# Kernel tuning notes

Measured on AMD Instinct MI355X. Metric: run time of the kernel, lower is better.

Reference implementation:

```python
import jax, jax.numpy as jnp
import numpy as np

EPS = 1e-6  # torch F.pairwise_distance default eps added to the difference


def setup_inputs() -> dict:
    key = jax.random.key(0)
    k1, k2 = jax.random.split(key)
    N, D = 8192, 256
    embeddings = jax.random.normal(k1, (N, D), dtype=jnp.float32)
    labels = jax.random.randint(k2, (N,), 0, 64, dtype=jnp.int32)
    return {"embeddings": embeddings, "labels": labels}


def reference(embeddings, labels):
    # Fused replacement for the O(N^2) python loop:
    # dist[i,j] = ||e_i - e_j + EPS||_2 (torch pairwise_distance semantics)
    #           = sqrt(||e_i||^2 + ||e_j||^2 - 2 e_i.e_j + 2*EPS*(sum(e_i)-sum(e_j)) + D*EPS^2)
    N, D = embeddings.shape
    sq_norm = jnp.sum(embeddings * embeddings, axis=-1)        # (N,)
    row_sum = jnp.sum(embeddings, axis=-1)                     # (N,)
    gram = embeddings @ embeddings.T                           # (N, N)
    sq = (sq_norm[:, None] + sq_norm[None, :] - 2.0 * gram
          + 2.0 * EPS * (row_sum[:, None] - row_sum[None, :])
          + D * EPS * EPS)
    dist = jnp.sqrt(jnp.maximum(sq, 0.0))                      # (N, N)
    mask = labels[:, None] == labels[None, :]                  # (N, N) bool
    loss = jnp.sum(jnp.where(mask, dist, 0.0)) / (N * (N - 1))
    return loss
```

## Files before the change

### kernel.cpp

```cpp
#include <hip/hip_runtime.h>
#include <stdint.h>


#define NROWS 8192
#define DDIM 256
#define NLAB 64
#define NTILEB (NLAB * 3)

typedef __attribute__((ext_vector_type(8))) short bfrag8;
typedef __attribute__((ext_vector_type(4))) float f32x4;

__device__ __forceinline__ unsigned short f2bf(float f) {
  unsigned u = __float_as_uint(f);
  u += 0x7FFFu + ((u >> 16) & 1u);
  return (unsigned short)(u >> 16);
}

__global__ void __launch_bounds__(512)
k_fused(const float* __restrict__ E, const int* __restrict__ lab,
        float* __restrict__ partials) {
  __shared__ __align__(16) char As[128 * 512];
  __shared__ __align__(16) char Bs[128 * 512];
  __shared__ int rowlistS[256];
  __shared__ float qAS[128], qBS[128];
  __shared__ int wcntS[8];
  __shared__ float wsum[8];

  const int bid = blockIdx.x;
  const int g = bid / 3, p = bid % 3;
  const int t = threadIdx.x, l = t & 63, w = t >> 6;
  const int tit = (p == 2) ? 1 : 0, tjt = (p == 0) ? 0 : 1;
  const bool diag = (p != 1);

  int lv[16];
  #pragma unroll
  for (int i = 0; i < 16; ++i)
    lv[i] = lab[(w * 16 + i) * 64 + l];

  int cntw = 0;
  #pragma unroll
  for (int i = 0; i < 16; ++i)
    cntw += (int)__popcll(__ballot(lv[i] == g));
  if (l == 0) wcntS[w] = cntw;
  if (t == 0) rowlistS[0] = 0;
  __syncthreads();
  int n_total = 0, base = 0;
  #pragma unroll
  for (int w2 = 0; w2 < 8; ++w2) {
    const int c = wcntS[w2];
    n_total += c;
    base += (w2 < w) ? c : 0;
  }
  #pragma unroll
  for (int i = 0; i < 16; ++i) {
    const unsigned long long m = __ballot(lv[i] == g);
    if (lv[i] == g) {
      const int rank = base + (int)__popcll(m & ((1ull << l) - 1ull));
      if (rank < 256) rowlistS[rank] = (w * 16 + i) * 64 + l;
    }
    base += (int)__popcll(m);
  }
  const int n = min(n_total, 256);
  __syncthreads();

  float blocksum = 0.f;
  const bool empty = (p != 0 && n <= 128);
  if (!empty) {
    const int gsw = l >> 1;
    const int half8 = (l & 1) * 8;
    if (diag) {
      #pragma unroll 8
      for (int r8 = 0; r8 < 16; ++r8) {
        const int r = w * 16 + r8;
        const int li = tit * 128 + r;
        const int grow = rowlistS[(li < n) ? li : 0];
        const float4 v = *reinterpret_cast<const float4*>(E + (size_t)grow * DDIM + l * 4);
        ushort4 b4;
        b4.x = f2bf(v.x); b4.y = f2bf(v.y); b4.z = f2bf(v.z); b4.w = f2bf(v.w);
        *reinterpret_cast<ushort4*>(
            As + r * 512 + ((gsw ^ (r & 15)) << 4) + half8) = b4;
      }
    } else {
      #pragma unroll 8
      for (int r8 = 0; r8 < 16; ++r8) {
        const int r = w * 16 + r8;
        const int growA = rowlistS[(r < n) ? r : 0];
        const int growB = rowlistS[(128 + r < n) ? 128 + r : 0];
        const float4 va = *reinterpret_cast<const float4*>(E + (size_t)growA * DDIM + l * 4);
        const float4 vb = *reinterpret_cast<const float4*>(E + (size_t)growB * DDIM + l * 4);
        ushort4 ba, bb;
        ba.x = f2bf(va.x); ba.y = f2bf(va.y); ba.z = f2bf(va.z); ba.w = f2bf(va.w);
        bb.x = f2bf(vb.x); bb.y = f2bf(vb.y); bb.z = f2bf(vb.z); bb.w = f2bf(vb.w);
        const int off = r * 512 + ((gsw ^ (r & 15)) << 4) + half8;
        *reinterpret_cast<ushort4*>(As + off) = ba;
        *reinterpret_cast<ushort4*>(Bs + off) = bb;
      }
    }
    __syncthreads();

    if (diag) {
      const int r = t >> 2, q4 = t & 3;
      float q = 0.f;
      #pragma unroll
      for (int i = 0; i < 8; ++i) {
        const int gidx = q4 * 8 + i;
        const bfrag8 v = *reinterpret_cast<const bfrag8*>(
            As + r * 512 + ((gidx ^ (r & 15)) << 4));
        #pragma unroll
        for (int e = 0; e < 8; ++e) {
          const float f = __uint_as_float(((unsigned)(unsigned short)v[e]) << 16);
          q = fmaf(f, f, q);
        }
      }
      q += __shfl_xor(q, 1);
      q += __shfl_xor(q, 2);
      if ((t & 3) == 0) qAS[r] = q;
    } else {
      const int rAll = t >> 1, hf = t & 1;
      const int r = rAll & 127;
      const char* buf = (rAll < 128) ? As : Bs;
      float q = 0.f;
      #pragma unroll
      for (int i = 0; i < 16; ++i) {
        const int gidx = hf * 16 + i;
        const bfrag8 v = *reinterpret_cast<const bfrag8*>(
            buf + r * 512 + ((gidx ^ (r & 15)) << 4));
        #pragma unroll
        for (int e = 0; e < 8; ++e) {
          const float f = __uint_as_float(((unsigned)(unsigned short)v[e]) << 16);
          q = fmaf(f, f, q);
        }
      }
      q += __shfl_xor(q, 1);
      if (hf == 0) { if (rAll < 128) qAS[r] = q; else qBS[r] = q; }
    }

    const char* Bbuf = diag ? As : Bs;
    const float* qBp = diag ? qAS : qBS;
    const int wr = w >> 2, wc = w & 3;
    const int colsel = l & 15;
    const int ksel = l >> 4;

    f32x4 acc[4][2];
    const f32x4 zero = {0.f, 0.f, 0.f, 0.f};
    #pragma unroll
    for (int m = 0; m < 4; ++m)
      #pragma unroll
      for (int nn = 0; nn < 2; ++nn)
        acc[m][nn] = zero;

    #pragma unroll
    for (int kk = 0; kk < 8; ++kk) {
      bfrag8 af[4], bf[2];
      #pragma unroll
      for (int m = 0; m < 4; ++m) {
        const int row = wr * 64 + m * 16 + colsel;
        const int gidx = (kk * 4 + ksel) ^ (row & 15);
        af[m] = *reinterpret_cast<const bfrag8*>(As + row * 512 + (gidx << 4));
      }
      #pragma unroll
      for (int nn = 0; nn < 2; ++nn) {
        const int row = wc * 32 + nn * 16 + colsel;
        const int gidx = (kk * 4 + ksel) ^ (row & 15);
        bf[nn] = *reinterpret_cast<const bfrag8*>(Bbuf + row * 512 + (gidx << 4));
      }
      #pragma unroll
      for (int m = 0; m < 4; ++m)
        #pragma unroll
        for (int nn = 0; nn < 2; ++nn)
          acc[m][nn] = __builtin_amdgcn_mfma_f32_16x16x32_bf16(af[m], bf[nn],
                                                               acc[m][nn], 0, 0, 0);
    }
    __syncthreads();

    float lsum = 0.f;
    #pragma unroll
    for (int m = 0; m < 4; ++m) {
      const int ib = wr * 64 + m * 16 + ksel * 4;
      const float q0 = qAS[ib], q1 = qAS[ib + 1], q2 = qAS[ib + 2], q3 = qAS[ib + 3];
      const int li = tit * 128 + ib;
      #pragma unroll
      for (int nn = 0; nn < 2; ++nn) {
        const int jb = wc * 32 + nn * 16 + colsel;
        const int lj = tjt * 128 + jb;
        const bool jv = lj < n;
        const float qj = qBp[jb];
        const f32x4 a = acc[m][nn];
        const float d0 = __builtin_amdgcn_sqrtf(fmaxf(q0 + qj - 2.f * a[0], 0.f));
        const float d1 = __builtin_amdgcn_sqrtf(fmaxf(q1 + qj - 2.f * a[1], 0.f));
        const float d2 = __builtin_amdgcn_sqrtf(fmaxf(q2 + qj - 2.f * a[2], 0.f));
        const float d3 = __builtin_amdgcn_sqrtf(fmaxf(q3 + qj - 2.f * a[3], 0.f));
        if (jv) {
          lsum += (li + 0 < n && li + 0 != lj) ? d0 : 0.f;
          lsum += (li + 1 < n && li + 1 != lj) ? d1 : 0.f;
          lsum += (li + 2 < n && li + 2 != lj) ? d2 : 0.f;
          lsum += (li + 3 < n && li + 3 != lj) ? d3 : 0.f;
        }
      }
    }
    #pragma unroll
    for (int o = 32; o; o >>= 1) lsum += __shfl_down(lsum, o);
    if (l == 0) wsum[w] = lsum;
    __syncthreads();
    const float wgt = (p == 1) ? 2.0f : 1.0f;
    blocksum = wgt * (wsum[0] + wsum[1] + wsum[2] + wsum[3] +
                      wsum[4] + wsum[5] + wsum[6] + wsum[7]);
  }

  if (t == 0) partials[bid] = blocksum;
}

__global__ void __launch_bounds__(64)
k_final(const float* __restrict__ partials, float* __restrict__ out, double invn) {
  const int l = threadIdx.x;
  double s = (double)partials[l] + (double)partials[l + 64] +
             (double)partials[l + 128];
  #pragma unroll
  for (int o = 32; o; o >>= 1) s += __shfl_down(s, o);
  if (l == 0) out[0] = (float)(s * invn);
}

extern "C" void kernel_launch(void* const* d_in, const int* in_sizes, int n_in,
                              void* d_out, int out_size, void* d_ws, size_t ws_size,
                              hipStream_t stream) {
  const float* E = (const float*)d_in[0];
  const int* lab = (const int*)d_in[1];
  float* out = (float*)d_out;
  (void)n_in; (void)in_sizes; (void)out_size; (void)ws_size;

  float* partials = (float*)d_ws;

  const double invn = 1.0 / ((double)NROWS * (double)(NROWS - 1));
  k_fused<<<NTILEB, 512, 0, stream>>>(E, lab, partials);
  k_final<<<1, 64, 0, stream>>>(partials, out, invn);
}
```

Before: 16.17 us.

## Split off-diagonal label tile across two blocks and fuse norms into staging

```diff
diff --git a/kernel.cpp b/kernel.cpp
--- a/kernel.cpp
+++ b/kernel.cpp
@@ -5,7 +5,7 @@
 #define NROWS 8192
 #define DDIM 256
 #define NLAB 64
-#define NTILEB (NLAB * 3)
+#define NBLK (NLAB * 4)
 
 typedef __attribute__((ext_vector_type(8))) short bfrag8;
 typedef __attribute__((ext_vector_type(4))) float f32x4;
@@ -14,6 +14,10 @@
   unsigned u = __float_as_uint(f);
   u += 0x7FFFu + ((u >> 16) & 1u);
   return (unsigned short)(u >> 16);
+}
+
+__device__ __forceinline__ float bf2f(unsigned short h) {
+  return __uint_as_float(((unsigned)h) << 16);
 }
 
 __global__ void __launch_bounds__(512)
@@ -27,10 +31,11 @@
   __shared__ float wsum[8];
 
   const int bid = blockIdx.x;
-  const int g = bid / 3, p = bid % 3;
+  const int g = bid >> 2, p = bid & 3;
   const int t = threadIdx.x, l = t & 63, w = t >> 6;
-  const int tit = (p == 2) ? 1 : 0, tjt = (p == 0) ? 0 : 1;
-  const bool diag = (p != 1);
+  const bool diag = (p < 2);
+  const int a0 = (p == 1) ? 128 : ((p == 3) ? 64 : 0);
+  const int b0 = (p == 0) ? 0 : 128;
 
   int lv[16];
   #pragma unroll
@@ -64,147 +69,188 @@
   __syncthreads();
 
   float blocksum = 0.f;
-  const bool empty = (p != 0 && n <= 128);
-  if (!empty) {
+  const bool active = (a0 < n) && (b0 < n);
+  if (active) {
     const int gsw = l >> 1;
     const int half8 = (l & 1) * 8;
     if (diag) {
       #pragma unroll 8
       for (int r8 = 0; r8 < 16; ++r8) {
         const int r = w * 16 + r8;
-        const int li = tit * 128 + r;
-        const int grow = rowlistS[(li < n) ? li : 0];
+        const int gi = a0 + r;
+        const int grow = rowlistS[(gi < n) ? gi : 0];
         const float4 v = *reinterpret_cast<const float4*>(E + (size_t)grow * DDIM + l * 4);
         ushort4 b4;
         b4.x = f2bf(v.x); b4.y = f2bf(v.y); b4.z = f2bf(v.z); b4.w = f2bf(v.w);
         *reinterpret_cast<ushort4*>(
             As + r * 512 + ((gsw ^ (r & 15)) << 4) + half8) = b4;
+        const float f0 = bf2f(b4.x), f1 = bf2f(b4.y);
+        const float f2 = bf2f(b4.z), f3 = bf2f(b4.w);
+        float q = f0 * f0 + f1 * f1 + f2 * f2 + f3 * f3;
+        #pragma unroll
+        for (int o = 32; o; o >>= 1) q += __shfl_down(q, o);
+        if (l == 0) qAS[r] = q;
       }
     } else {
+      #pragma unroll 8
+      for (int r8 = 0; r8 < 8; ++r8) {
+        const int r = w * 8 + r8;
+        const int gi = a0 + r;
+        const int grow = rowlistS[(gi < n) ? gi : 0];
+        const float4 v = *reinterpret_cast<const float4*>(E + (size_t)grow * DDIM + l * 4);
+        ushort4 b4;
+        b4.x = f2bf(v.x); b4.y = f2bf(v.y); b4.z = f2bf(v.z); b4.w = f2bf(v.w);
+        *reinterpret_cast<ushort4*>(
+            As + r * 512 + ((gsw ^ (r & 15)) << 4) + half8) = b4;
+        const float f0 = bf2f(b4.x), f1 = bf2f(b4.y);
+        const float f2 = bf2f(b4.z), f3 = bf2f(b4.w);
+        float q = f0 * f0 + f1 * f1 + f2 * f2 + f3 * f3;
+        #pragma unroll
+        for (int o = 32; o; o >>= 1) q += __shfl_down(q, o);
+        if (l == 0) qAS[r] = q;
+      }
       #pragma unroll 8
       for (int r8 = 0; r8 < 16; ++r8) {
         const int r = w * 16 + r8;
-        const int growA = rowlistS[(r < n) ? r : 0];
-        const int growB = rowlistS[(128 + r < n) ? 128 + r : 0];
-        const float4 va = *reinterpret_cast<const float4*>(E + (size_t)growA * DDIM + l * 4);
-        const float4 vb = *reinterpret_cast<const float4*>(E + (size_t)growB * DDIM + l * 4);
-        ushort4 ba, bb;
-        ba.x = f2bf(va.x); ba.y = f2bf(va.y); ba.z = f2bf(va.z); ba.w = f2bf(va.w);
-        bb.x = f2bf(vb.x); bb.y = f2bf(vb.y); bb.z = f2bf(vb.z); bb.w = f2bf(vb.w);
-        const int off = r * 512 + ((gsw ^ (r & 15)) << 4) + half8;
-        *reinterpret_cast<ushort4*>(As + off) = ba;
-        *reinterpret_cast<ushort4*>(Bs + off) = bb;
+        const int gj = 128 + r;
+        const int grow = rowlistS[(gj < n) ? gj : 0];
+        const float4 v = *reinterpret_cast<const float4*>(E + (size_t)grow * DDIM + l * 4);
+        ushort4 b4;
+        b4.x = f2bf(v.x); b4.y = f2bf(v.y); b4.z = f2bf(v.z); b4.w = f2bf(v.w);
+        *reinterpret_cast<ushort4*>(
+            Bs + r * 512 + ((gsw ^ (r & 15)) << 4) + half8) = b4;
+        const float f0 = bf2f(b4.x), f1 = bf2f(b4.y);
+        const float f2 = bf2f(b4.z), f3 = bf2f(b4.w);
+        float q = f0 * f0 + f1 * f1 + f2 * f2 + f3 * f3;
+        #pragma unroll
+        for (int o = 32; o; o >>= 1) q += __shfl_down(q, o);
+        if (l == 0) qBS[r] = q;
       }
     }
     __syncthreads();
 
-    if (diag) {
-      const int r = t >> 2, q4 = t & 3;
-      float q = 0.f;
-      #pragma unroll
-      for (int i = 0; i < 8; ++i) {
-        const int gidx = q4 * 8 + i;
-        const bfrag8 v = *reinterpret_cast<const bfrag8*>(
-            As + r * 512 + ((gidx ^ (r & 15)) << 4));
-        #pragma unroll
-        for (int e = 0; e < 8; ++e) {
-          const float f = __uint_as_float(((unsigned)(unsigned short)v[e]) << 16);
-          q = fmaf(f, f, q);
-        }
-      }
-      q += __shfl_xor(q, 1);
-      q += __shfl_xor(q, 2);
-      if ((t & 3) == 0) qAS[r] = q;
-    } else {
-      const int rAll = t >> 1, hf = t & 1;
-      const int r = rAll & 127;
-      const char* buf = (rAll < 128) ? As : Bs;
-      float q = 0.f;
-      #pragma unroll
-      for (int i = 0; i < 16; ++i) {
-        const int gidx = hf * 16 + i;
-        const bfrag8 v = *reinterpret_cast<const bfrag8*>(
-            buf + r * 512 + ((gidx ^ (r & 15)) << 4));
-        #pragma unroll
-        for (int e = 0; e < 8; ++e) {
-          const float f = __uint_as_float(((unsigned)(unsigned short)v[e]) << 16);
-          q = fmaf(f, f, q);
-        }
-      }
-      q += __shfl_xor(q, 1);
-      if (hf == 0) { if (rAll < 128) qAS[r] = q; else qBS[r] = q; }
-    }
-
-    const char* Bbuf = diag ? As : Bs;
-    const float* qBp = diag ? qAS : qBS;
-    const int wr = w >> 2, wc = w & 3;
     const int colsel = l & 15;
     const int ksel = l >> 4;
-
-    f32x4 acc[4][2];
-    const f32x4 zero = {0.f, 0.f, 0.f, 0.f};
-    #pragma unroll
-    for (int m = 0; m < 4; ++m)
-      #pragma unroll
-      for (int nn = 0; nn < 2; ++nn)
-        acc[m][nn] = zero;
-
-    #pragma unroll
-    for (int kk = 0; kk < 8; ++kk) {
-      bfrag8 af[4], bf[2];
+    const int wr = w >> 2, wc = w & 3;
+    float lsum = 0.f;
+
+    if (diag) {
+      f32x4 acc[4][2];
+      const f32x4 zero = {0.f, 0.f, 0.f, 0.f};
+      #pragma unroll
+      for (int m = 0; m < 4; ++m)
+        #pragma unroll
+        for (int nn = 0; nn < 2; ++nn)
+          acc[m][nn] = zero;
+      #pragma unroll
+      for (int kk = 0; kk < 8; ++kk) {
+        bfrag8 af[4], bf[2];
+        #pragma unroll
+        for (int m = 0; m < 4; ++m) {
+          const int row = wr * 64 + m * 16 + colsel;
+          const int gidx = (kk * 4 + ksel) ^ (row & 15);
+          af[m] = *reinterpret_cast<const bfrag8*>(As + row * 512 + (gidx << 4));
+        }
+        #pragma unroll
+        for (int nn = 0; nn < 2; ++nn) {
+          const int row = wc * 32 + nn * 16 + colsel;
+          const int gidx = (kk * 4 + ksel) ^ (row & 15);
+          bf[nn] = *reinterpret_cast<const bfrag8*>(As + row * 512 + (gidx << 4));
+        }
+        #pragma unroll
+        for (int m = 0; m < 4; ++m)
+          #pragma unroll
+          for (int nn = 0; nn < 2; ++nn)
+            acc[m][nn] = __builtin_amdgcn_mfma_f32_16x16x32_bf16(af[m], bf[nn],
+                                                                 acc[m][nn], 0, 0, 0);
+      }
       #pragma unroll
       for (int m = 0; m < 4; ++m) {
-        const int row = wr * 64 + m * 16 + colsel;
-        const int gidx = (kk * 4 + ksel) ^ (row & 15);
-        af[m] = *reinterpret_cast<const bfrag8*>(As + row * 512 + (gidx << 4));
-      }
-      #pragma unroll
-      for (int nn = 0; nn < 2; ++nn) {
-        const int row = wc * 32 + nn * 16 + colsel;
-        const int gidx = (kk * 4 + ksel) ^ (row & 15);
-        bf[nn] = *reinterpret_cast<const bfrag8*>(Bbuf + row * 512 + (gidx << 4));
-      }
-      #pragma unroll
-      for (int m = 0; m < 4; ++m)
+        const int ib = wr * 64 + m * 16 + ksel * 4;
+        const int gi = a0 + ib;
+        const float q0 = qAS[ib], q1 = qAS[ib + 1], q2 = qAS[ib + 2], q3 = qAS[ib + 3];
+        #pragma unroll
+        for (int nn = 0; nn < 2; ++nn) {
+          const int jb = wc * 32 + nn * 16 + colsel;
+          const int gj = a0 + jb;
+          const bool jv = gj < n;
+          const float qj = qAS[jb];
+          const f32x4 a = acc[m][nn];
+          const float d0 = __builtin_amdgcn_sqrtf(fmaxf(q0 + qj - 2.f * a[0], 0.f));
+          const float d1 = __builtin_amdgcn_sqrtf(fmaxf(q1 + qj - 2.f * a[1], 0.f));
+          const float d2 = __builtin_amdgcn_sqrtf(fmaxf(q2 + qj - 2.f * a[2], 0.f));
+          const float d3 = __builtin_amdgcn_sqrtf(fmaxf(q3 + qj - 2.f * a[3], 0.f));
+          if (jv) {
+            lsum += (gi + 0 < n && gi + 0 != gj) ? d0 : 0.f;
+            lsum += (gi + 1 < n && gi + 1 != gj) ? d1 : 0.f;
+            lsum += (gi + 2 < n && gi + 2 != gj) ? d2 : 0.f;
+            lsum += (gi + 3 < n && gi + 3 != gj) ? d3 : 0.f;
+          }
+        }
+      }
+    } else {
+      f32x4 acc[2][2];
+      const f32x4 zero = {0.f, 0.f, 0.f, 0.f};
+      #pragma unroll
+      for (int m = 0; m < 2; ++m)
         #pragma unroll
         for (int nn = 0; nn < 2; ++nn)
-          acc[m][nn] = __builtin_amdgcn_mfma_f32_16x16x32_bf16(af[m], bf[nn],
-                                                               acc[m][nn], 0, 0, 0);
+          acc[m][nn] = zero;
+      #pragma unroll
+      for (int kk = 0; kk < 8; ++kk) {
+        bfrag8 af[2], bf[2];
+        #pragma unroll
+        for (int m = 0; m < 2; ++m) {
+          const int row = wr * 32 + m * 16 + colsel;
+          const int gidx = (kk * 4 + ksel) ^ (row & 15);
+          af[m] = *reinterpret_cast<const bfrag8*>(As + row * 512 + (gidx << 4));
+        }
+        #pragma unroll
+        for (int nn = 0; nn < 2; ++nn) {
+          const int row = wc * 32 + nn * 16 + colsel;
+          const int gidx = (kk * 4 + ksel) ^ (row & 15);
+          bf[nn] = *reinterpret_cast<const bfrag8*>(Bs + row * 512 + (gidx << 4));
+        }
+        #pragma unroll
+        for (int m = 0; m < 2; ++m)
+          #pragma unroll
+          for (int nn = 0; nn < 2; ++nn)
+            acc[m][nn] = __builtin_amdgcn_mfma_f32_16x16x32_bf16(af[m], bf[nn],
+                                                                 acc[m][nn], 0, 0, 0);
+      }
+      #pragma unroll
+      for (int m = 0; m < 2; ++m) {
+        const int ib = wr * 32 + m * 16 + ksel * 4;
+        const int gi = a0 + ib;
+        const float q0 = qAS[ib], q1 = qAS[ib + 1], q2 = qAS[ib + 2], q3 = qAS[ib + 3];
+        #pragma unroll
+        for (int nn = 0; nn < 2; ++nn) {
+          const int jb = wc * 32 + nn * 16 + colsel;
+          const int gj = 128 + jb;
+          const bool jv = gj < n;
+          const float qj = qBS[jb];
+          const f32x4 a = acc[m][nn];
+          const float d0 = __builtin_amdgcn_sqrtf(fmaxf(q0 + qj - 2.f * a[0], 0.f));
+          const float d1 = __builtin_amdgcn_sqrtf(fmaxf(q1 + qj - 2.f * a[1], 0.f));
+          const float d2 = __builtin_amdgcn_sqrtf(fmaxf(q2 + qj - 2.f * a[2], 0.f));
+          const float d3 = __builtin_amdgcn_sqrtf(fmaxf(q3 + qj - 2.f * a[3], 0.f));
+          if (jv) {
+            lsum += (gi + 0 < n) ? d0 : 0.f;
+            lsum += (gi + 1 < n) ? d1 : 0.f;
+            lsum += (gi + 2 < n) ? d2 : 0.f;
+            lsum += (gi + 3 < n) ? d3 : 0.f;
+          }
+        }
+      }
+      lsum *= 2.0f;
     }
-    __syncthreads();
-
-    float lsum = 0.f;
-    #pragma unroll
-    for (int m = 0; m < 4; ++m) {
-      const int ib = wr * 64 + m * 16 + ksel * 4;
-      const float q0 = qAS[ib], q1 = qAS[ib + 1], q2 = qAS[ib + 2], q3 = qAS[ib + 3];
-      const int li = tit * 128 + ib;
-      #pragma unroll
-      for (int nn = 0; nn < 2; ++nn) {
-        const int jb = wc * 32 + nn * 16 + colsel;
-        const int lj = tjt * 128 + jb;
-        const bool jv = lj < n;
-        const float qj = qBp[jb];
-        const f32x4 a = acc[m][nn];
-        const float d0 = __builtin_amdgcn_sqrtf(fmaxf(q0 + qj - 2.f * a[0], 0.f));
-        const float d1 = __builtin_amdgcn_sqrtf(fmaxf(q1 + qj - 2.f * a[1], 0.f));
-        const float d2 = __builtin_amdgcn_sqrtf(fmaxf(q2 + qj - 2.f * a[2], 0.f));
-        const float d3 = __builtin_amdgcn_sqrtf(fmaxf(q3 + qj - 2.f * a[3], 0.f));
-        if (jv) {
-          lsum += (li + 0 < n && li + 0 != lj) ? d0 : 0.f;
-          lsum += (li + 1 < n && li + 1 != lj) ? d1 : 0.f;
-          lsum += (li + 2 < n && li + 2 != lj) ? d2 : 0.f;
-          lsum += (li + 3 < n && li + 3 != lj) ? d3 : 0.f;
-        }
-      }
-    }
+
     #pragma unroll
     for (int o = 32; o; o >>= 1) lsum += __shfl_down(lsum, o);
     if (l == 0) wsum[w] = lsum;
     __syncthreads();
-    const float wgt = (p == 1) ? 2.0f : 1.0f;
-    blocksum = wgt * (wsum[0] + wsum[1] + wsum[2] + wsum[3] +
-                      wsum[4] + wsum[5] + wsum[6] + wsum[7]);
+    blocksum = wsum[0] + wsum[1] + wsum[2] + wsum[3] +
+               wsum[4] + wsum[5] + wsum[6] + wsum[7];
   }
 
   if (t == 0) partials[bid] = blocksum;
@@ -214,7 +260,7 @@
 k_final(const float* __restrict__ partials, float* __restrict__ out, double invn) {
   const int l = threadIdx.x;
   double s = (double)partials[l] + (double)partials[l + 64] +
-             (double)partials[l + 128];
+             (double)partials[l + 128] + (double)partials[l + 192];
   #pragma unroll
   for (int o = 32; o; o >>= 1) s += __shfl_down(s, o);
   if (l == 0) out[0] = (float)(s * invn);
@@ -231,6 +277,6 @@
   float* partials = (float*)d_ws;
 
   const double invn = 1.0 / ((double)NROWS * (double)(NROWS - 1));
-  k_fused<<<NTILEB, 512, 0, stream>>>(E, lab, partials);
+  k_fused<<<NBLK, 512, 0, stream>>>(E, lab, partials);
   k_final<<<1, 64, 0, stream>>>(partials, out, invn);
 }
```

Result: slower. 21.68 us (+34.1%).
